# Kernel tuning notes

Hardware: AMD Instinct MI355X
Metric: run time of the kernel (lower is better)

The kernel has to match this reference:

```python
import jax, jax.numpy as jnp
import numpy as np

N_NODES = 50000
N_EDGES = 800000
OBS_DIM = 25
HID = 128
EMB = 64
EDGE_DIM = 8
HEADS = 4
N_LAYERS = 3
COMM_RANGE = 1500.0
LN_EPS = 1e-5


def layernorm(x, g, b):
    mu = jnp.mean(x, axis=-1, keepdims=True)
    var = jnp.mean((x - mu) ** 2, axis=-1, keepdims=True)
    return (x - mu) / jnp.sqrt(var + LN_EPS) * g + b


def setup_inputs() -> dict:
    key = jax.random.key(0)
    ks = iter(jax.random.split(key, 64))

    def w(shape, s=0.05):
        return (jax.random.normal(next(ks), shape, jnp.float32) * s).astype(jnp.float32)

    inp = {}
    inp["observations"] = jax.random.normal(next(ks), (N_NODES, OBS_DIM), jnp.float32)
    inp["positions"] = jax.random.uniform(next(ks), (N_NODES, 2), jnp.float32) * 1000.0
    inp["edge_index"] = jax.random.randint(next(ks), (2, N_EDGES), 0, N_NODES, jnp.int32)
    # node encoder (obs_encoder branch: Linear-LN-ReLU-Linear-ReLU)
    inp["enc_w1"] = w((OBS_DIM, HID)); inp["enc_b1"] = w((HID,), 0.01)
    inp["enc_ln_g"] = jnp.ones((HID,), jnp.float32); inp["enc_ln_b"] = jnp.zeros((HID,), jnp.float32)
    inp["enc_w2"] = w((HID, EMB)); inp["enc_b2"] = w((EMB,), 0.01)
    cat_dim = 2 * EMB + EDGE_DIM  # 136
    # per-layer GNN params, stacked over layers
    inp["msg_w1"] = w((N_LAYERS, cat_dim, HID)); inp["msg_b1"] = w((N_LAYERS, HID), 0.01)
    inp["msg_w2"] = w((N_LAYERS, HID, EMB)); inp["msg_b2"] = w((N_LAYERS, EMB), 0.01)
    inp["att_w1"] = w((N_LAYERS, cat_dim, HID)); inp["att_b1"] = w((N_LAYERS, HID), 0.01)
    inp["att_w2"] = w((N_LAYERS, HID, HEADS)); inp["att_b2"] = w((N_LAYERS, HEADS), 0.01)
    inp["upd_w1"] = w((N_LAYERS, 2 * EMB, HID)); inp["upd_b1"] = w((N_LAYERS, HID), 0.01)
    inp["upd_w2"] = w((N_LAYERS, HID, EMB)); inp["upd_b2"] = w((N_LAYERS, EMB), 0.01)
    inp["ln_g"] = jnp.ones((N_LAYERS, EMB), jnp.float32); inp["ln_b"] = jnp.zeros((N_LAYERS, EMB), jnp.float32)
    # output projection
    inp["out_w1"] = w((EMB, HID)); inp["out_b1"] = w((HID,), 0.01)
    inp["out_w2"] = w((HID, EMB)); inp["out_b2"] = w((EMB,), 0.01)
    return inp


def reference(observations, positions, edge_index,
              enc_w1, enc_b1, enc_ln_g, enc_ln_b, enc_w2, enc_b2,
              msg_w1, msg_b1, msg_w2, msg_b2,
              att_w1, att_b1, att_w2, att_b2,
              upd_w1, upd_b1, upd_w2, upd_b2,
              ln_g, ln_b,
              out_w1, out_b1, out_w2, out_b2):
    n = observations.shape[0]
    # --- node encoder (use_full_obs=True path) ---
    h = observations @ enc_w1 + enc_b1
    h = jax.nn.relu(layernorm(h, enc_ln_g, enc_ln_b))
    x = jax.nn.relu(h @ enc_w2 + enc_b2)  # [N, EMB]

    # --- edge features (build_graph math, edges given) ---
    src, dst = edge_index[0], edge_index[1]
    rel = positions[dst] - positions[src]                    # [E, 2]
    dist = jnp.linalg.norm(rel, axis=-1, keepdims=True)      # [E, 1]
    rel_n = rel / (dist + 1e-6)
    dist_n = dist / COMM_RANGE
    angle = jnp.arctan2(rel[:, 1], rel[:, 0])[:, None]
    edge_attr = jnp.concatenate(
        [dist_n, rel_n, jnp.cos(angle), jnp.sin(angle), dist_n ** 2,
         jnp.zeros((rel.shape[0], 2), x.dtype)], axis=-1)    # [E, 8]

    # --- GNN communication layers (PyG: x_i = target = dst, x_j = source = src,
    #     aggregate to dst; dropout inactive at inference) ---
    for l in range(N_LAYERS):
        cat = jnp.concatenate([x[dst], x[src], edge_attr], axis=-1)       # [E, 136]
        m = jax.nn.relu(cat @ msg_w1[l] + msg_b1[l]) @ msg_w2[l] + msg_b2[l]   # [E, EMB]
        a = jax.nn.relu(cat @ att_w1[l] + att_b1[l]) @ att_w2[l] + att_b2[l]   # [E, HEADS]
        wgt = jnp.mean(jax.nn.softmax(a, axis=-1), axis=-1, keepdims=True)     # [E, 1]
        aggr = jax.ops.segment_sum(m * wgt, dst, num_segments=n)               # [N, EMB]
        upd_in = jnp.concatenate([x, aggr], axis=-1)                            # [N, 2*EMB]
        upd = jax.nn.relu(upd_in @ upd_w1[l] + upd_b1[l]) @ upd_w2[l] + upd_b2[l]
        x = layernorm(x + upd, ln_g[l], ln_b[l])

    # --- output projection ---
    return jax.nn.relu(x @ out_w1 + out_b1) @ out_w2 + out_b2
```

## Files before the change

### kernel.cpp

```cpp
#include <hip/hip_runtime.h>
#include <hip/hip_bf16.h>

typedef unsigned short ushort_t;
typedef unsigned int uint_t;

constexpr int OBS  = 25;
constexpr int HID  = 128;
constexpr int EMB  = 64;
constexpr int CAT  = 136;
constexpr int NN   = 50000;

constexpr int TE      = 256;
constexpr int ETHR    = 512;
constexpr int K1PAD   = 152;
constexpr int K2PAD   = 140;
constexpr int K1STEPS = 9;
constexpr int K2STEPS = 8;

constexpr int TB = 128;

typedef __attribute__((ext_vector_type(8)))  short bf16x8;
typedef __attribute__((ext_vector_type(16))) float f32x16;

__device__ __forceinline__ ushort_t f2bf(float f) {
    union { float f; uint_t u; } v; v.f = f;
    uint_t r = v.u + 0x7FFFu + ((v.u >> 16) & 1u);
    return (ushort_t)(r >> 16);
}

__device__ __forceinline__ bf16x8 ld8(const ushort_t* p) {
    uint2 lo = *reinterpret_cast<const uint2*>(p);
    uint2 hi = *reinterpret_cast<const uint2*>(p + 4);
    uint4 u = make_uint4(lo.x, lo.y, hi.x, hi.y);
    return __builtin_bit_cast(bf16x8, u);
}

#define CROW(R, LHI) (4 * (LHI) + ((R) & 3) + 8 * ((R) >> 2))

__global__ __launch_bounds__(256) void k_hist(
    const int* __restrict__ dst, int* __restrict__ hist, int ne)
{
    int e = blockIdx.x * 256 + threadIdx.x;
    if (e < ne) atomicAdd(&hist[dst[e]], 1);
}

__global__ __launch_bounds__(512) void k_scan1(
    const int* __restrict__ hist, int* __restrict__ scanned,
    int* __restrict__ bsum, int nn)
{
    __shared__ int s[512];
    int t = threadIdx.x, i = blockIdx.x * 512 + t;
    int v = (i < nn) ? hist[i] : 0;
    s[t] = v; __syncthreads();
#pragma unroll
    for (int off = 1; off < 512; off <<= 1) {
        int x = (t >= off) ? s[t - off] : 0;
        __syncthreads();
        s[t] += x;
        __syncthreads();
    }
    if (i < nn) scanned[i] = s[t] - v;
    if (t == 511) bsum[blockIdx.x] = s[511];
}

__global__ void k_scan2(int* __restrict__ bsum, int nb)
{
    if (blockIdx.x == 0 && threadIdx.x == 0) {
        int run = 0;
        for (int b = 0; b < nb; ++b) { int t = bsum[b]; bsum[b] = run; run += t; }
    }
}

__global__ __launch_bounds__(512) void k_scan3(
    int* __restrict__ scanned, const int* __restrict__ bsum, int nn)
{
    int i = blockIdx.x * 512 + threadIdx.x;
    if (i < nn) scanned[i] += bsum[blockIdx.x];
}

__global__ __launch_bounds__(256) void k_scatter_feat(
    const float* __restrict__ pos, const int* __restrict__ src,
    const int* __restrict__ dst, int* __restrict__ ofs,
    uint4* __restrict__ eab4, int ne)
{
    int e = blockIdx.x * 256 + threadIdx.x;
    if (e >= ne) return;
    int s = src[e], d = dst[e];
    float rx = pos[d * 2 + 0] - pos[s * 2 + 0];
    float ry = pos[d * 2 + 1] - pos[s * 2 + 1];
    float dist = sqrtf(rx * rx + ry * ry);
    float inv = 1.f / (dist + 1e-6f);
    float dn = dist * (1.f / 1500.f);
    uint_t ux = (uint_t)f2bf(dn) | ((uint_t)f2bf(rx * inv) << 16);
    uint_t uy = (uint_t)f2bf(ry * inv) | ((dist > 0.f ? 0u : 1u) << 16);
    int p = atomicAdd(&ofs[d], 1);
    eab4[p] = make_uint4(ux, uy, (uint_t)s, (uint_t)d);
}

__global__ __launch_bounds__(256) void k_prep(
    const float* __restrict__ w1, const float* __restrict__ w2,
    ushort_t* __restrict__ w1t, ushort_t* __restrict__ w2t)
{
    int t = blockIdx.x * 256 + threadIdx.x;
    const int n1 = 3 * HID * K1PAD;
    if (t < n1) {
        int l = t / (HID * K1PAD), rem = t % (HID * K1PAD);
        int c = rem / K1PAD, k = rem % K1PAD;
        float v = (k < CAT) ? w1[(size_t)l * CAT * HID + (size_t)k * HID + c] : 0.f;
        w1t[t] = f2bf(v);
    }
    const int n2 = 3 * EMB * K2PAD;
    if (t < n2) {
        int l = t / (EMB * K2PAD), rem = t % (EMB * K2PAD);
        int c = rem / K2PAD, k = rem % K2PAD;
        float v = (k < HID) ? w2[(size_t)l * HID * EMB + (size_t)k * EMB + c] : 0.f;
        w2t[t] = f2bf(v);
    }
}

constexpr int EKP = 36;
__global__ __launch_bounds__(256, 1) void k_encoder_mfma(
    const float* __restrict__ obs,
    const float* __restrict__ w1, const float* __restrict__ b1,
    const float* __restrict__ lng, const float* __restrict__ lnb,
    const float* __restrict__ w2, const float* __restrict__ b2,
    float* __restrict__ x, ushort_t* __restrict__ xb, int n)
{
    __shared__ __align__(16) ushort_t s_OB[TB * EKP];
    __shared__ __align__(16) ushort_t s_B1[HID * EKP];
    __shared__ __align__(16) float    s_G[TB * 132];
    __shared__ __align__(16) ushort_t s_H[TB * K2PAD];
    __shared__ __align__(16) ushort_t s_W2[EMB * K2PAD];

    const int tid = threadIdx.x;
    const int lane = tid & 63, wid = tid >> 6;
    const int wr = wid >> 1, wc = wid & 1;
    const int l31 = lane & 31, lhi = lane >> 5;
    const int n0 = blockIdx.x * TB;

    for (int i = tid; i < TB * 32; i += 256) {
        int row = i >> 5, k = i & 31;
        int gn = n0 + row;
        float v = (gn < n && k < OBS) ? obs[(size_t)gn * OBS + k] : 0.f;
        s_OB[row * EKP + k] = f2bf(v);
    }
    for (int i = tid; i < 32 * HID; i += 256) {
        int k = i >> 7, c = i & 127;
        float v = (k < OBS) ? w1[k * HID + c] : 0.f;
        s_B1[c * EKP + k] = f2bf(v);
    }
    __syncthreads();

    f32x16 a00, a01, a10, a11;
    {
        float bv0 = b1[wc * 64 + l31], bv1 = b1[wc * 64 + 32 + l31];
#pragma unroll
        for (int i = 0; i < 16; ++i) { a00[i] = bv0; a01[i] = bv1; a10[i] = bv0; a11[i] = bv1; }
    }
    {
        const ushort_t* aR0 = s_OB + (wr * 64 + l31) * EKP;
        const ushort_t* aR1 = aR0 + 32 * EKP;
        const ushort_t* bR0 = s_B1 + (wc * 64 + l31) * EKP;
        const ushort_t* bR1 = bR0 + 32 * EKP;
        const int koff = lhi * 8;
#pragma unroll
        for (int s = 0; s < 2; ++s) {
            const int ke = s * 16 + koff;
            bf16x8 av0 = ld8(aR0 + ke), av1 = ld8(aR1 + ke);
            bf16x8 bv0 = ld8(bR0 + ke), bv1 = ld8(bR1 + ke);
            a00 = __builtin_amdgcn_mfma_f32_32x32x16_bf16(av0, bv0, a00, 0, 0, 0);
            a01 = __builtin_amdgcn_mfma_f32_32x32x16_bf16(av0, bv1, a01, 0, 0, 0);
            a10 = __builtin_amdgcn_mfma_f32_32x32x16_bf16(av1, bv0, a10, 0, 0, 0);
            a11 = __builtin_amdgcn_mfma_f32_32x32x16_bf16(av1, bv1, a11, 0, 0, 0);
        }
    }
#define WRITE_G(ACC, SUB, NC)                                                  \
    {                                                                          \
        const int col = wc * 64 + (NC) * 32 + l31;                             \
        _Pragma("unroll")                                                      \
        for (int r = 0; r < 16; ++r) {                                         \
            int row = wr * 64 + (SUB) * 32 + CROW(r, lhi);                     \
            s_G[row * 132 + col] = ACC[r];                                     \
        }                                                                      \
    }
    WRITE_G(a00, 0, 0) WRITE_G(a01, 0, 1) WRITE_G(a10, 1, 0) WRITE_G(a11, 1, 1)
#undef WRITE_G
    __syncthreads();

    for (int i = tid; i < HID * EMB; i += 256) {
        int k = i >> 6, c = i & 63;
        s_W2[c * K2PAD + k] = f2bf(w2[i]);
    }
    if (tid < TB) {
        float sum = 0.f, sum2 = 0.f;
        const float* gr = s_G + tid * 132;
#pragma unroll 8
        for (int q = 0; q < HID; ++q) { float v = gr[q]; sum += v; sum2 += v * v; }
        float mu = sum * (1.f / HID);
        float var = fmaxf(sum2 * (1.f / HID) - mu * mu, 0.f);
        float rs = 1.f / sqrtf(var + 1e-5f);
        ushort_t* hr = s_H + tid * K2PAD;
#pragma unroll 8
        for (int q = 0; q < HID; ++q) {
            float v = (gr[q] - mu) * rs * lng[q] + lnb[q];
            hr[q] = f2bf(fmaxf(v, 0.f));
        }
    }
    __syncthreads();

    f32x16 c0, c1;
    {
        float bv = b2[wc * 32 + l31];
#pragma unroll
        for (int i = 0; i < 16; ++i) { c0[i] = bv; c1[i] = bv; }
    }
    {
        const ushort_t* aR0 = s_H + (wr * 64 + l31) * K2PAD;
        const ushort_t* aR1 = aR0 + 32 * K2PAD;
        const ushort_t* bR = s_W2 + (wc * 32 + l31) * K2PAD;
        const int koff = lhi * 8;
#pragma unroll
        for (int s = 0; s < K2STEPS; ++s) {
            const int ke = s * 16 + koff;
            bf16x8 av0 = ld8(aR0 + ke), av1 = ld8(aR1 + ke);
            bf16x8 bv = ld8(bR + ke);
            c0 = __builtin_amdgcn_mfma_f32_32x32x16_bf16(av0, bv, c0, 0, 0, 0);
            c1 = __builtin_amdgcn_mfma_f32_32x32x16_bf16(av1, bv, c1, 0, 0, 0);
        }
    }
    {
        const int col = wc * 32 + l31;
#define STORE_X(CC, SUB)                                                       \
        {                                                                      \
            _Pragma("unroll")                                                  \
            for (int r = 0; r < 16; ++r) {                                     \
                int row = wr * 64 + (SUB) * 32 + CROW(r, lhi);                 \
                int gn = n0 + row;                                             \
                if (gn < n) {                                                  \
                    float v = fmaxf(CC[r], 0.f);                               \
                    x[(size_t)gn * EMB + col] = v;                             \
                    xb[(size_t)gn * EMB + col] = f2bf(v);                      \
                }                                                              \
            }                                                                  \
        }
        STORE_X(c0, 0) STORE_X(c1, 1)
#undef STORE_X
    }
}

__global__ __launch_bounds__(ETHR, 4) void k_edge_mfma(
    const ushort_t* __restrict__ xb,
    const uint4* __restrict__ eab4,
    const ushort_t* __restrict__ w1t,
    const float* __restrict__ b1,
    const ushort_t* __restrict__ w2t,
    const float* __restrict__ b2,
    float* __restrict__ aggr, int ne)
{
    __shared__ __align__(16) ushort_t s_A[TE * K1PAD];
    __shared__ int s_dst[TE];
    ushort_t* s_H = s_A;
    float*    s_M = reinterpret_cast<float*>(s_A);

    const int tid  = threadIdx.x;
    const int lane = tid & 63, wid = tid >> 6;
    const int wr = wid >> 1, wc = wid & 1;
    const int l31 = lane & 31, lhi = lane >> 5;

    const int nwg = ne / TE;
    const int q = nwg >> 3, rr = nwg & 7;
    const int bid = blockIdx.x;
    const int xcd = bid & 7, loc = bid >> 3;
    const int swz = (xcd < rr ? xcd * (q + 1) : rr * (q + 1) + (xcd - rr) * q) + loc;
    const int e0 = swz * TE;

    {
        const int e = tid >> 1, h = tid & 1, ge = e0 + e;
        ushort_t* arow = s_A + e * K1PAD;
        uint4 ev = eab4[ge];
        if (h == 0) {
            s_dst[e] = (int)ev.w;
            const uint4* sp = reinterpret_cast<const uint4*>(xb + (size_t)ev.w * EMB);
            uint4* dp = reinterpret_cast<uint4*>(arow);
#pragma unroll
            for (int i = 0; i < 8; ++i) dp[i] = sp[i];
        } else {
            const uint4* sp = reinterpret_cast<const uint4*>(xb + (size_t)ev.z * EMB);
            uint4* dp = reinterpret_cast<uint4*>(arow + EMB);
#pragma unroll
            for (int i = 0; i < 8; ++i) dp[i] = sp[i];
            uint_t dn_b = ev.x & 0xFFFFu, rxn_b = ev.x >> 16;
            uint_t ryn_b = ev.y & 0xFFFFu, flag = ev.y >> 16;
            uint_t cos_b = flag ? 0x3F80u : rxn_b;
            uint_t sin_b = flag ? 0u : ryn_b;
            union { uint_t u; float f; } cv; cv.u = dn_b << 16;
            uint_t dn2_b = (uint_t)f2bf(cv.f * cv.f);
            uint4* fp4 = reinterpret_cast<uint4*>(arow + 2 * EMB);
            fp4[0] = make_uint4(dn_b | (rxn_b << 16), ryn_b | (cos_b << 16),
                                sin_b | (dn2_b << 16), 0u);
            uint4* pp = reinterpret_cast<uint4*>(arow + CAT);
            pp[0] = make_uint4(0u, 0u, 0u, 0u);
            pp[1] = make_uint4(0u, 0u, 0u, 0u);
        }
    }
    __syncthreads();

    f32x16 a00, a01, a10, a11;
    {
        float bv0 = b1[wc * 64 + l31], bv1 = b1[wc * 64 + 32 + l31];
#pragma unroll
        for (int i = 0; i < 16; ++i) { a00[i] = bv0; a01[i] = bv1; a10[i] = bv0; a11[i] = bv1; }
    }
    {
        const ushort_t* aR0 = s_A + (wr * 64 + l31) * K1PAD;
        const ushort_t* aR1 = aR0 + 32 * K1PAD;
        const ushort_t* bR0 = w1t + (wc * 64 + l31) * K1PAD;
        const ushort_t* bR1 = bR0 + 32 * K1PAD;
        const int koff = lhi * 8;
#pragma unroll
        for (int s = 0; s < K1STEPS; ++s) {
            const int ke = s * 16 + koff;
            bf16x8 av0 = ld8(aR0 + ke);
            bf16x8 av1 = ld8(aR1 + ke);
            bf16x8 bv0 = ld8(bR0 + ke);
            bf16x8 bv1 = ld8(bR1 + ke);
            a00 = __builtin_amdgcn_mfma_f32_32x32x16_bf16(av0, bv0, a00, 0, 0, 0);
            a01 = __builtin_amdgcn_mfma_f32_32x32x16_bf16(av0, bv1, a01, 0, 0, 0);
            a10 = __builtin_amdgcn_mfma_f32_32x32x16_bf16(av1, bv0, a10, 0, 0, 0);
            a11 = __builtin_amdgcn_mfma_f32_32x32x16_bf16(av1, bv1, a11, 0, 0, 0);
        }
    }
    __syncthreads();

#define WRITE_H(ACC, SUB, NC)                                                  \
    {                                                                          \
        const int col = wc * 64 + (NC) * 32 + l31;                             \
        _Pragma("unroll")                                                      \
        for (int r = 0; r < 16; ++r) {                                         \
            int row = wr * 64 + (SUB) * 32 + CROW(r, lhi);                     \
            s_H[row * K2PAD + col] = f2bf(fmaxf(ACC[r], 0.f));                 \
        }                                                                      \
    }
    WRITE_H(a00, 0, 0) WRITE_H(a01, 0, 1) WRITE_H(a10, 1, 0) WRITE_H(a11, 1, 1)
#undef WRITE_H
    __syncthreads();

    f32x16 c0, c1;
    {
        float bv = b2[wc * 32 + l31];
#pragma unroll
        for (int i = 0; i < 16; ++i) { c0[i] = bv; c1[i] = bv; }
    }
    {
        const ushort_t* aR0 = s_H + (wr * 64 + l31) * K2PAD;
        const ushort_t* aR1 = aR0 + 32 * K2PAD;
        const ushort_t* bR = w2t + (wc * 32 + l31) * K2PAD;
        const int koff = lhi * 8;
#pragma unroll
        for (int s = 0; s < K2STEPS; ++s) {
            const int ke = s * 16 + koff;
            bf16x8 av0 = ld8(aR0 + ke);
            bf16x8 av1 = ld8(aR1 + ke);
            bf16x8 bv = ld8(bR + ke);
            c0 = __builtin_amdgcn_mfma_f32_32x32x16_bf16(av0, bv, c0, 0, 0, 0);
            c1 = __builtin_amdgcn_mfma_f32_32x32x16_bf16(av1, bv, c1, 0, 0, 0);
        }
    }
    __syncthreads();

    {
        const int col = wc * 32 + l31;
#pragma unroll
        for (int r = 0; r < 16; ++r) {
            int row = wr * 64 + CROW(r, lhi);
            s_M[row * 68 + col] = c0[r] * 0.25f;
            s_M[(row + 32) * 68 + col] = c1[r] * 0.25f;
        }
    }
    __syncthreads();

    if (tid < 256) {
        const int col = tid & 63, grp = tid >> 6, base = grp * 64;
        int cur = s_dst[base];
        int runstart = 0;
        float acc = 0.f;
#pragma unroll 4
        for (int r = 0; r < 64; ++r) {
            int d = s_dst[base + r];
            float v = s_M[(base + r) * 68 + col];
            if (d != cur) {
                float* p = aggr + (size_t)cur * EMB + col;
                if (runstart == 0) atomicAdd(p, acc);
                else *p = acc;
                acc = 0.f; cur = d; runstart = r;
            }
            acc += v;
        }
        atomicAdd(aggr + (size_t)cur * EMB + col, acc);
    }
}

__global__ __launch_bounds__(256, 2) void k_update_mfma(
    float* __restrict__ x, ushort_t* __restrict__ xb,
    const float* __restrict__ aggr,
    const float* __restrict__ w1, const float* __restrict__ b1,
    const float* __restrict__ w2, const float* __restrict__ b2,
    const float* __restrict__ g, const float* __restrict__ bb, int n)
{
    __shared__ __align__(16) ushort_t s_A[TB * K2PAD];
    __shared__ __align__(16) ushort_t s_B[TB * K2PAD];
    ushort_t* s_H  = s_A;
    ushort_t* s_W2 = s_B;
    float*    s_U  = reinterpret_cast<float*>(s_B);

    const int tid = threadIdx.x;
    const int lane = tid & 63, wid = tid >> 6;
    const int wr = wid >> 1, wc = wid & 1;
    const int l31 = lane & 31, lhi = lane >> 5;
    const int n0 = blockIdx.x * TB;

    {
        const int row = tid >> 1, h = tid & 1;
        const int gn = n0 + row;
        ushort_t* arow = s_A + row * K2PAD;
        if (h == 0) {
            uint2* dp = reinterpret_cast<uint2*>(arow);
            if (gn < n) {
                const uint2* sp = reinterpret_cast<const uint2*>(xb + (size_t)gn * EMB);
#pragma unroll
                for (int i = 0; i < 16; ++i) dp[i] = sp[i];
            } else {
                const uint2 z = make_uint2(0u, 0u);
#pragma unroll
                for (int i = 0; i < 16; ++i) dp[i] = z;
            }
        } else {
            if (gn < n) {
                const float4* sp = reinterpret_cast<const float4*>(aggr + (size_t)gn * EMB);
#pragma unroll
                for (int i = 0; i < 16; ++i) {
                    float4 v = sp[i];
                    ushort_t* qq = arow + EMB + i * 4;
                    qq[0] = f2bf(v.x); qq[1] = f2bf(v.y); qq[2] = f2bf(v.z); qq[3] = f2bf(v.w);
                }
            } else {
#pragma unroll
                for (int i = 0; i < 16; ++i) {
                    ushort_t* qq = arow + EMB + i * 4;
                    qq[0] = 0; qq[1] = 0; qq[2] = 0; qq[3] = 0;
                }
            }
        }
    }
    for (int i = tid; i < 128 * 128; i += 256) {
        int k = i >> 7, c = i & 127;
        s_B[c * K2PAD + k] = f2bf(w1[i]);
    }
    __syncthreads();

    f32x16 a00, a01, a10, a11;
    {
        float bv0 = b1[wc * 64 + l31], bv1 = b1[wc * 64 + 32 + l31];
#pragma unroll
        for (int i = 0; i < 16; ++i) { a00[i] = bv0; a01[i] = bv1; a10[i] = bv0; a11[i] = bv1; }
    }
    {
        const ushort_t* aR0 = s_A + (wr * 64 + l31) * K2PAD;
        const ushort_t* aR1 = aR0 + 32 * K2PAD;
        const ushort_t* bR0 = s_B + (wc * 64 + l31) * K2PAD;
        const ushort_t* bR1 = bR0 + 32 * K2PAD;
        const int koff = lhi * 8;
#pragma unroll
        for (int s = 0; s < K2STEPS; ++s) {
            const int ke = s * 16 + koff;
            bf16x8 av0 = ld8(aR0 + ke), av1 = ld8(aR1 + ke);
            bf16x8 bv0 = ld8(bR0 + ke), bv1 = ld8(bR1 + ke);
            a00 = __builtin_amdgcn_mfma_f32_32x32x16_bf16(av0, bv0, a00, 0, 0, 0);
            a01 = __builtin_amdgcn_mfma_f32_32x32x16_bf16(av0, bv1, a01, 0, 0, 0);
            a10 = __builtin_amdgcn_mfma_f32_32x32x16_bf16(av1, bv0, a10, 0, 0, 0);
            a11 = __builtin_amdgcn_mfma_f32_32x32x16_bf16(av1, bv1, a11, 0, 0, 0);
        }
    }
    __syncthreads();

#define WRITE_H(ACC, SUB, NC)                                                  \
    {                                                                          \
        const int col = wc * 64 + (NC) * 32 + l31;                             \
        _Pragma("unroll")                                                      \
        for (int r = 0; r < 16; ++r) {                                         \
            int row = wr * 64 + (SUB) * 32 + CROW(r, lhi);                     \
            s_H[row * K2PAD + col] = f2bf(fmaxf(ACC[r], 0.f));                 \
        }                                                                      \
    }
    WRITE_H(a00, 0, 0) WRITE_H(a01, 0, 1) WRITE_H(a10, 1, 0) WRITE_H(a11, 1, 1)
#undef WRITE_H
    for (int i = tid; i < HID * EMB; i += 256) {
        int k = i >> 6, c = i & 63;
        s_W2[c * K2PAD + k] = f2bf(w2[i]);
    }
    __syncthreads();

    f32x16 c0, c1;
    {
        float bv = b2[wc * 32 + l31];
#pragma unroll
        for (int i = 0; i < 16; ++i) { c0[i] = bv; c1[i] = bv; }
    }
    {
        const ushort_t* aR0 = s_H + (wr * 64 + l31) * K2PAD;
        const ushort_t* aR1 = aR0 + 32 * K2PAD;
        const ushort_t* bR = s_W2 + (wc * 32 + l31) * K2PAD;
        const int koff = lhi * 8;
#pragma unroll
        for (int s = 0; s < K2STEPS; ++s) {
            const int ke = s * 16 + koff;
            bf16x8 av0 = ld8(aR0 + ke), av1 = ld8(aR1 + ke);
            bf16x8 bv = ld8(bR + ke);
            c0 = __builtin_amdgcn_mfma_f32_32x32x16_bf16(av0, bv, c0, 0, 0, 0);
            c1 = __builtin_amdgcn_mfma_f32_32x32x16_bf16(av1, bv, c1, 0, 0, 0);
        }
    }
    __syncthreads();

    {
        const int col = wc * 32 + l31;
#pragma unroll
        for (int r = 0; r < 16; ++r) {
            int row = wr * 64 + CROW(r, lhi);
            s_U[row * 68 + col] = c0[r];
            s_U[(row + 32) * 68 + col] = c1[r];
        }
    }
    __syncthreads();

    if (tid < TB) {
        int gn = n0 + tid;
        if (gn < n) {
            const float* xr = x + (size_t)gn * EMB;
            float* ur = s_U + tid * 68;
            float sum = 0.f, sum2 = 0.f;
#pragma unroll 8
            for (int q = 0; q < EMB; ++q) {
                float v = xr[q] + ur[q];
                ur[q] = v;
                sum += v; sum2 += v * v;
            }
            float mu = sum * (1.f / EMB);
            float var = fmaxf(sum2 * (1.f / EMB) - mu * mu, 0.f);
            float rs = 1.f / sqrtf(var + 1e-5f);
            float* xo = x + (size_t)gn * EMB;
            ushort_t* xbo = xb + (size_t)gn * EMB;
#pragma unroll 8
            for (int q = 0; q < EMB; ++q) {
                float v = (ur[q] - mu) * rs * g[q] + bb[q];
                xo[q] = v;
                xbo[q] = f2bf(v);
            }
        }
    }
}

constexpr int OKP = 68;
__global__ __launch_bounds__(256, 2) void k_output_mfma(
    const ushort_t* __restrict__ xb,
    const float* __restrict__ w1, const float* __restrict__ b1,
    const float* __restrict__ w2, const float* __restrict__ b2,
    float* __restrict__ out, int n)
{
    __shared__ __align__(16) ushort_t s_A[TB * OKP];
    __shared__ __align__(16) ushort_t s_B[HID * OKP];
    __shared__ __align__(16) ushort_t s_H[TB * K2PAD];
    __shared__ __align__(16) ushort_t s_W2[EMB * K2PAD];

    const int tid = threadIdx.x;
    const int lane = tid & 63, wid = tid >> 6;
    const int wr = wid >> 1, wc = wid & 1;
    const int l31 = lane & 31, lhi = lane >> 5;
    const int n0 = blockIdx.x * TB;

    for (int i = tid; i < TB * 16; i += 256) {
        int row = i >> 4, q = i & 15;
        int gn = n0 + row;
        uint2 v = make_uint2(0u, 0u);
        if (gn < n) v = reinterpret_cast<const uint2*>(xb + (size_t)gn * EMB)[q];
        *reinterpret_cast<uint2*>(s_A + row * OKP + q * 4) = v;
    }
    for (int i = tid; i < EMB * HID; i += 256) {
        int k = i >> 7, c = i & 127;
        s_B[c * OKP + k] = f2bf(w1[i]);
    }
    for (int i = tid; i < HID * EMB; i += 256) {
        int k = i >> 6, c = i & 63;
        s_W2[c * K2PAD + k] = f2bf(w2[i]);
    }
    __syncthreads();

    f32x16 a00, a01, a10, a11;
    {
        float bv0 = b1[wc * 64 + l31], bv1 = b1[wc * 64 + 32 + l31];
#pragma unroll
        for (int i = 0; i < 16; ++i) { a00[i] = bv0; a01[i] = bv1; a10[i] = bv0; a11[i] = bv1; }
    }
    {
        const ushort_t* aR0 = s_A + (wr * 64 + l31) * OKP;
        const ushort_t* aR1 = aR0 + 32 * OKP;
        const ushort_t* bR0 = s_B + (wc * 64 + l31) * OKP;
        const ushort_t* bR1 = bR0 + 32 * OKP;
        const int koff = lhi * 8;
#pragma unroll
        for (int s = 0; s < 4; ++s) {
            const int ke = s * 16 + koff;
            bf16x8 av0 = ld8(aR0 + ke), av1 = ld8(aR1 + ke);
            bf16x8 bv0 = ld8(bR0 + ke), bv1 = ld8(bR1 + ke);
            a00 = __builtin_amdgcn_mfma_f32_32x32x16_bf16(av0, bv0, a00, 0, 0, 0);
            a01 = __builtin_amdgcn_mfma_f32_32x32x16_bf16(av0, bv1, a01, 0, 0, 0);
            a10 = __builtin_amdgcn_mfma_f32_32x32x16_bf16(av1, bv0, a10, 0, 0, 0);
            a11 = __builtin_amdgcn_mfma_f32_32x32x16_bf16(av1, bv1, a11, 0, 0, 0);
        }
    }
    __syncthreads();

#define WRITE_H(ACC, SUB, NC)                                                  \
    {                                                                          \
        const int col = wc * 64 + (NC) * 32 + l31;                             \
        _Pragma("unroll")                                                      \
        for (int r = 0; r < 16; ++r) {                                         \
            int row = wr * 64 + (SUB) * 32 + CROW(r, lhi);                     \
            s_H[row * K2PAD + col] = f2bf(fmaxf(ACC[r], 0.f));                 \
        }                                                                      \
    }
    WRITE_H(a00, 0, 0) WRITE_H(a01, 0, 1) WRITE_H(a10, 1, 0) WRITE_H(a11, 1, 1)
#undef WRITE_H
    __syncthreads();

    f32x16 c0, c1;
    {
        float bv = b2[wc * 32 + l31];
#pragma unroll
        for (int i = 0; i < 16; ++i) { c0[i] = bv; c1[i] = bv; }
    }
    {
        const ushort_t* aR0 = s_H + (wr * 64 + l31) * K2PAD;
        const ushort_t* aR1 = aR0 + 32 * K2PAD;
        const ushort_t* bR = s_W2 + (wc * 32 + l31) * K2PAD;
        const int koff = lhi * 8;
#pragma unroll
        for (int s = 0; s < K2STEPS; ++s) {
            const int ke = s * 16 + koff;
            bf16x8 av0 = ld8(aR0 + ke), av1 = ld8(aR1 + ke);
            bf16x8 bv = ld8(bR + ke);
            c0 = __builtin_amdgcn_mfma_f32_32x32x16_bf16(av0, bv, c0, 0, 0, 0);
            c1 = __builtin_amdgcn_mfma_f32_32x32x16_bf16(av1, bv, c1, 0, 0, 0);
        }
    }
    {
        const int col = wc * 32 + l31;
#pragma unroll
        for (int r = 0; r < 16; ++r) {
            int row0 = wr * 64 + CROW(r, lhi);
            int g0 = n0 + row0, g1 = g0 + 32;
            if (g0 < n) out[(size_t)g0 * EMB + col] = c0[r];
            if (g1 < n) out[(size_t)g1 * EMB + col] = c1[r];
        }
    }
}

extern "C" void kernel_launch(void* const* d_in, const int* in_sizes, int n_in,
                              void* d_out, int out_size, void* d_ws, size_t ws_size,
                              hipStream_t stream)
{
    const float* obs     = (const float*)d_in[0];
    const float* pos     = (const float*)d_in[1];
    const int*   eidx    = (const int*)d_in[2];
    const float* enc_w1  = (const float*)d_in[3];
    const float* enc_b1  = (const float*)d_in[4];
    const float* enc_lng = (const float*)d_in[5];
    const float* enc_lnb = (const float*)d_in[6];
    const float* enc_w2  = (const float*)d_in[7];
    const float* enc_b2  = (const float*)d_in[8];
    const float* msg_w1  = (const float*)d_in[9];
    const float* msg_b1  = (const float*)d_in[10];
    const float* msg_w2  = (const float*)d_in[11];
    const float* msg_b2  = (const float*)d_in[12];
    const float* upd_w1  = (const float*)d_in[17];
    const float* upd_b1  = (const float*)d_in[18];
    const float* upd_w2  = (const float*)d_in[19];
    const float* upd_b2  = (const float*)d_in[20];
    const float* ln_g    = (const float*)d_in[21];
    const float* ln_b    = (const float*)d_in[22];
    const float* out_w1  = (const float*)d_in[23];
    const float* out_b1  = (const float*)d_in[24];
    const float* out_w2  = (const float*)d_in[25];
    const float* out_b2  = (const float*)d_in[26];

    const int n  = in_sizes[0] / OBS;
    const int ne = in_sizes[2] / 2;
    const int* src = eidx;
    const int* dst = eidx + ne;

    char* ws = (char*)d_ws;
    float*    x     = (float*)ws;
    ushort_t* xbuf  = (ushort_t*)(ws + 12800000);
    uint4*    eab4  = (uint4*)(ws + 19200000);
    float*    aggr  = (float*)(ws + 32000000);
    ushort_t* w1t   = (ushort_t*)(ws + 44800000);
    ushort_t* w2t   = (ushort_t*)(ws + 44916736);
    int*      hist  = (int*)(ws + 44970496);
    int*      scan  = (int*)(ws + 45170496);
    int*      bsum  = (int*)(ws + 45370496);

    const int NB1 = (NN + 511) / 512;
    const int nb  = (n + TB - 1) / TB;

    hipMemsetAsync(hist, 0, NN * sizeof(int), stream);
    k_hist<<<(ne + 255) / 256, 256, 0, stream>>>(dst, hist, ne);
    k_scan1<<<NB1, 512, 0, stream>>>(hist, scan, bsum, NN);
    k_scan2<<<1, 64, 0, stream>>>(bsum, NB1);
    k_scan3<<<NB1, 512, 0, stream>>>(scan, bsum, NN);
    k_scatter_feat<<<(ne + 255) / 256, 256, 0, stream>>>(pos, src, dst, scan,
                                                         eab4, ne);

    k_prep<<<(3 * HID * K1PAD + 255) / 256, 256, 0, stream>>>(msg_w1, msg_w2, w1t, w2t);
    k_encoder_mfma<<<nb, 256, 0, stream>>>(obs, enc_w1, enc_b1, enc_lng, enc_lnb,
                                           enc_w2, enc_b2, x, xbuf, n);

    for (int l = 0; l < 3; ++l) {
        hipMemsetAsync(aggr, 0, (size_t)n * EMB * sizeof(float), stream);
        k_edge_mfma<<<ne / TE, ETHR, 0, stream>>>(
            xbuf, eab4,
            w1t + (size_t)l * HID * K1PAD, msg_b1 + (size_t)l * HID,
            w2t + (size_t)l * EMB * K2PAD, msg_b2 + (size_t)l * EMB,
            aggr, ne);
        k_update_mfma<<<nb, 256, 0, stream>>>(
            x, xbuf, aggr,
            upd_w1 + (size_t)l * 2 * EMB * HID, upd_b1 + (size_t)l * HID,
            upd_w2 + (size_t)l * HID * EMB, upd_b2 + (size_t)l * EMB,
            ln_g + (size_t)l * EMB, ln_b + (size_t)l * EMB, n);
    }
    k_output_mfma<<<nb, 256, 0, stream>>>(
        xbuf, out_w1, out_b1, out_w2, out_b2, (float*)d_out, n);
}
```

Before: 820.7 us.

## Sort edges by source half then destination, shrink edge tiles, add nontemporal memory ops

Edges are now bucketed by a composite key (source half, destination), so each tile gathers source rows from only half of the node table, which should improve cache locality for the source gathers. The edge tile shrinks from 256 edges and 512 threads to 128 and 256, with a smaller LDS padding, and the segmented reduction now always uses atomics. The scan drops its serial second kernel and instead has each block sum the preceding block totals itself. Nontemporal loads and stores are added for edge records and aggr reads. Destination runs are split into two buckets, which creates more atomic traffic, and the smaller tiles mean more launch and weight-load overhead.

```diff
diff --git a/kernel.cpp b/kernel.cpp
--- a/kernel.cpp
+++ b/kernel.cpp
@@ -9,10 +9,12 @@
 constexpr int EMB  = 64;
 constexpr int CAT  = 136;
 constexpr int NN   = 50000;
-
-constexpr int TE      = 256;
-constexpr int ETHR    = 512;
-constexpr int K1PAD   = 152;
+constexpr int HALF = NN / 2;
+constexpr int NK   = 2 * NN;
+
+constexpr int TE      = 128;
+constexpr int ETHR    = 256;
+constexpr int K1PAD   = 148;
 constexpr int K2PAD   = 140;
 constexpr int K1STEPS = 9;
 constexpr int K2STEPS = 8;
@@ -21,6 +23,8 @@
 
 typedef __attribute__((ext_vector_type(8)))  short bf16x8;
 typedef __attribute__((ext_vector_type(16))) float f32x16;
+typedef __attribute__((ext_vector_type(4)))  uint_t uint4v;
+typedef __attribute__((ext_vector_type(4)))  float f32x4;
 
 __device__ __forceinline__ ushort_t f2bf(float f) {
     union { float f; uint_t u; } v; v.f = f;
@@ -38,19 +42,23 @@
 #define CROW(R, LHI) (4 * (LHI) + ((R) & 3) + 8 * ((R) >> 2))
 
 __global__ __launch_bounds__(256) void k_hist(
-    const int* __restrict__ dst, int* __restrict__ hist, int ne)
+    const int* __restrict__ src, const int* __restrict__ dst,
+    int* __restrict__ hist, int ne)
 {
     int e = blockIdx.x * 256 + threadIdx.x;
-    if (e < ne) atomicAdd(&hist[dst[e]], 1);
+    if (e < ne) {
+        int key = (src[e] >= HALF ? NN : 0) + dst[e];
+        atomicAdd(&hist[key], 1);
+    }
 }
 
 __global__ __launch_bounds__(512) void k_scan1(
     const int* __restrict__ hist, int* __restrict__ scanned,
-    int* __restrict__ bsum, int nn)
+    int* __restrict__ bsum, int nk)
 {
     __shared__ int s[512];
     int t = threadIdx.x, i = blockIdx.x * 512 + t;
-    int v = (i < nn) ? hist[i] : 0;
+    int v = (i < nk) ? hist[i] : 0;
     s[t] = v; __syncthreads();
 #pragma unroll
     for (int off = 1; off < 512; off <<= 1) {
@@ -59,29 +67,28 @@
         s[t] += x;
         __syncthreads();
     }
-    if (i < nn) scanned[i] = s[t] - v;
+    if (i < nk) scanned[i] = s[t] - v;
     if (t == 511) bsum[blockIdx.x] = s[511];
 }
 
-__global__ void k_scan2(int* __restrict__ bsum, int nb)
-{
-    if (blockIdx.x == 0 && threadIdx.x == 0) {
+__global__ __launch_bounds__(512) void k_scan3(
+    int* __restrict__ scanned, const int* __restrict__ bsum, int nk)
+{
+    __shared__ int pref;
+    if (threadIdx.x == 0) {
         int run = 0;
-        for (int b = 0; b < nb; ++b) { int t = bsum[b]; bsum[b] = run; run += t; }
-    }
-}
-
-__global__ __launch_bounds__(512) void k_scan3(
-    int* __restrict__ scanned, const int* __restrict__ bsum, int nn)
-{
+        for (int b = 0; b < blockIdx.x; ++b) run += bsum[b];
+        pref = run;
+    }
+    __syncthreads();
     int i = blockIdx.x * 512 + threadIdx.x;
-    if (i < nn) scanned[i] += bsum[blockIdx.x];
+    if (i < nk) scanned[i] += pref;
 }
 
 __global__ __launch_bounds__(256) void k_scatter_feat(
     const float* __restrict__ pos, const int* __restrict__ src,
     const int* __restrict__ dst, int* __restrict__ ofs,
-    uint4* __restrict__ eab4, int ne)
+    uint4v* __restrict__ eab4, int ne)
 {
     int e = blockIdx.x * 256 + threadIdx.x;
     if (e >= ne) return;
@@ -93,8 +100,10 @@
     float dn = dist * (1.f / 1500.f);
     uint_t ux = (uint_t)f2bf(dn) | ((uint_t)f2bf(rx * inv) << 16);
     uint_t uy = (uint_t)f2bf(ry * inv) | ((dist > 0.f ? 0u : 1u) << 16);
-    int p = atomicAdd(&ofs[d], 1);
-    eab4[p] = make_uint4(ux, uy, (uint_t)s, (uint_t)d);
+    int key = (s >= HALF ? NN : 0) + d;
+    int p = atomicAdd(&ofs[key], 1);
+    uint4v ev = { ux, uy, (uint_t)s, (uint_t)d };
+    __builtin_nontemporal_store(ev, eab4 + p);
 }
 
 __global__ __launch_bounds__(256) void k_prep(
@@ -250,7 +259,7 @@
 
 __global__ __launch_bounds__(ETHR, 4) void k_edge_mfma(
     const ushort_t* __restrict__ xb,
-    const uint4* __restrict__ eab4,
+    const uint4v* __restrict__ eab4,
     const ushort_t* __restrict__ w1t,
     const float* __restrict__ b1,
     const ushort_t* __restrict__ w2t,
@@ -277,30 +286,30 @@
     {
         const int e = tid >> 1, h = tid & 1, ge = e0 + e;
         ushort_t* arow = s_A + e * K1PAD;
-        uint4 ev = eab4[ge];
+        uint4v ev = __builtin_nontemporal_load(eab4 + ge);
         if (h == 0) {
             s_dst[e] = (int)ev.w;
-            const uint4* sp = reinterpret_cast<const uint4*>(xb + (size_t)ev.w * EMB);
-            uint4* dp = reinterpret_cast<uint4*>(arow);
-#pragma unroll
-            for (int i = 0; i < 8; ++i) dp[i] = sp[i];
+            const uint2* sp = reinterpret_cast<const uint2*>(xb + (size_t)ev.w * EMB);
+            uint2* dp = reinterpret_cast<uint2*>(arow);
+#pragma unroll
+            for (int i = 0; i < 16; ++i) dp[i] = sp[i];
         } else {
-            const uint4* sp = reinterpret_cast<const uint4*>(xb + (size_t)ev.z * EMB);
-            uint4* dp = reinterpret_cast<uint4*>(arow + EMB);
-#pragma unroll
-            for (int i = 0; i < 8; ++i) dp[i] = sp[i];
+            const uint2* sp = reinterpret_cast<const uint2*>(xb + (size_t)ev.z * EMB);
+            uint2* dp = reinterpret_cast<uint2*>(arow + EMB);
+#pragma unroll
+            for (int i = 0; i < 16; ++i) dp[i] = sp[i];
             uint_t dn_b = ev.x & 0xFFFFu, rxn_b = ev.x >> 16;
             uint_t ryn_b = ev.y & 0xFFFFu, flag = ev.y >> 16;
             uint_t cos_b = flag ? 0x3F80u : rxn_b;
             uint_t sin_b = flag ? 0u : ryn_b;
             union { uint_t u; float f; } cv; cv.u = dn_b << 16;
             uint_t dn2_b = (uint_t)f2bf(cv.f * cv.f);
-            uint4* fp4 = reinterpret_cast<uint4*>(arow + 2 * EMB);
-            fp4[0] = make_uint4(dn_b | (rxn_b << 16), ryn_b | (cos_b << 16),
-                                sin_b | (dn2_b << 16), 0u);
-            uint4* pp = reinterpret_cast<uint4*>(arow + CAT);
-            pp[0] = make_uint4(0u, 0u, 0u, 0u);
-            pp[1] = make_uint4(0u, 0u, 0u, 0u);
+            uint2* ap = reinterpret_cast<uint2*>(arow + 2 * EMB);
+            ap[0] = make_uint2(dn_b | (rxn_b << 16), ryn_b | (cos_b << 16));
+            ap[1] = make_uint2(sin_b | (dn2_b << 16), 0u);
+            uint2* pp = reinterpret_cast<uint2*>(arow + CAT);
+            pp[0] = make_uint2(0u, 0u); pp[1] = make_uint2(0u, 0u);
+            pp[2] = make_uint2(0u, 0u);
         }
     }
     __syncthreads();
@@ -379,20 +388,17 @@
     }
     __syncthreads();
 
-    if (tid < 256) {
-        const int col = tid & 63, grp = tid >> 6, base = grp * 64;
+    {
+        const int col = tid & 63, g = tid >> 6, base = g * 32;
         int cur = s_dst[base];
-        int runstart = 0;
         float acc = 0.f;
-#pragma unroll 4
-        for (int r = 0; r < 64; ++r) {
+#pragma unroll 8
+        for (int r = 0; r < 32; ++r) {
             int d = s_dst[base + r];
             float v = s_M[(base + r) * 68 + col];
             if (d != cur) {
-                float* p = aggr + (size_t)cur * EMB + col;
-                if (runstart == 0) atomicAdd(p, acc);
-                else *p = acc;
-                acc = 0.f; cur = d; runstart = r;
+                atomicAdd(aggr + (size_t)cur * EMB + col, acc);
+                acc = 0.f; cur = d;
             }
             acc += v;
         }
@@ -436,10 +442,10 @@
             }
         } else {
             if (gn < n) {
-                const float4* sp = reinterpret_cast<const float4*>(aggr + (size_t)gn * EMB);
+                const f32x4* sp = reinterpret_cast<const f32x4*>(aggr + (size_t)gn * EMB);
 #pragma unroll
                 for (int i = 0; i < 16; ++i) {
-                    float4 v = sp[i];
+                    f32x4 v = __builtin_nontemporal_load(sp + i);
                     ushort_t* qq = arow + EMB + i * 4;
                     qq[0] = f2bf(v.x); qq[1] = f2bf(v.y); qq[2] = f2bf(v.z); qq[3] = f2bf(v.w);
                 }
@@ -701,22 +707,21 @@
     char* ws = (char*)d_ws;
     float*    x     = (float*)ws;
     ushort_t* xbuf  = (ushort_t*)(ws + 12800000);
-    uint4*    eab4  = (uint4*)(ws + 19200000);
+    uint4v*   eab4  = (uint4v*)(ws + 19200000);
     float*    aggr  = (float*)(ws + 32000000);
     ushort_t* w1t   = (ushort_t*)(ws + 44800000);
-    ushort_t* w2t   = (ushort_t*)(ws + 44916736);
-    int*      hist  = (int*)(ws + 44970496);
-    int*      scan  = (int*)(ws + 45170496);
-    int*      bsum  = (int*)(ws + 45370496);
-
-    const int NB1 = (NN + 511) / 512;
+    ushort_t* w2t   = (ushort_t*)(ws + 44913664);
+    int*      hist  = (int*)(ws + 44967424);
+    int*      scan  = (int*)(ws + 45367424);
+    int*      bsum  = (int*)(ws + 45767424);
+
+    const int NB1 = (NK + 511) / 512;
     const int nb  = (n + TB - 1) / TB;
 
-    hipMemsetAsync(hist, 0, NN * sizeof(int), stream);
-    k_hist<<<(ne + 255) / 256, 256, 0, stream>>>(dst, hist, ne);
-    k_scan1<<<NB1, 512, 0, stream>>>(hist, scan, bsum, NN);
-    k_scan2<<<1, 64, 0, stream>>>(bsum, NB1);
-    k_scan3<<<NB1, 512, 0, stream>>>(scan, bsum, NN);
+    hipMemsetAsync(hist, 0, NK * sizeof(int), stream);
+    k_hist<<<(ne + 255) / 256, 256, 0, stream>>>(src, dst, hist, ne);
+    k_scan1<<<NB1, 512, 0, stream>>>(hist, scan, bsum, NK);
+    k_scan3<<<NB1, 512, 0, stream>>>(scan, bsum, NK);
     k_scatter_feat<<<(ne + 255) / 256, 256, 0, stream>>>(pos, src, dst, scan,
                                                          eab4, ne);
 
```

Result: faster. 795.3 us (-3.1%).
